# Kernel optimization log

Measured on AMD Instinct MI355X. Metric: run time of the kernel, lower is better.

Reference implementation:

```python
import jax, jax.numpy as jnp
import numpy as np

N = 16384; T = 65536; H = 128; G = 512; E = 65536; NEI = 32768
NIT = 4  # num_interactions
NL = 4   # finaldepth (hidden layers after the first)
EPS = 1e-5
INV = float(1.0 / np.sqrt(1.0 + EPS))  # fresh BatchNorm1d in eval mode: running_mean=0, running_var=1


def _bn(x, g, b):
    # eval-mode BatchNorm with mean=0, var=1: (x - 0)/sqrt(1+eps)*gamma + beta
    return x * (g * INV) + b


def setup_inputs() -> dict:
    key = jax.random.key(0)
    ks = jax.random.split(key, 16)
    inp = {}
    inp["node_positions"] = jax.random.normal(ks[0], (N, 2), jnp.float32)
    inp["edge_index_2rd"] = jax.random.randint(ks[1], (3, T), 0, N)  # (i, j, k) triplets
    inp["edx_jk"] = jax.random.randint(ks[2], (T,), 0, E)
    inp["edx_ij"] = jax.random.randint(ks[3], (T,), 0, E)
    inp["num_edge_inside"] = NEI
    inp["node_to_feature"] = jax.random.randint(ks[4], (N,), 0, G)
    # mlp_geo: Linear(3, H) + BN
    inp["Wg"] = jax.random.normal(ks[5], (3, H), jnp.float32) / np.sqrt(3.0)
    inp["bg"] = jnp.zeros((H,), jnp.float32)
    inp["gamg"] = 1.0 + 0.1 * jax.random.normal(ks[6], (H,), jnp.float32)
    inp["betg"] = 0.1 * jax.random.normal(ks[7], (H,), jnp.float32)
    # per-interaction (NIT), per-edge-type-group (4) MLPs
    inp["W0"] = jax.random.normal(ks[8], (NIT, 4, 4 * H, H), jnp.float32) / np.sqrt(4.0 * H)
    inp["b0"] = jnp.zeros((NIT, 4, H), jnp.float32)
    inp["g0"] = 1.0 + 0.1 * jax.random.normal(ks[9], (NIT, 4, H), jnp.float32)
    inp["be0"] = 0.1 * jax.random.normal(ks[10], (NIT, 4, H), jnp.float32)
    inp["Wh"] = jax.random.normal(ks[11], (NIT, NL, 4, H, H), jnp.float32) / np.sqrt(float(H))
    inp["bh"] = jnp.zeros((NIT, NL, 4, H), jnp.float32)
    inp["gh"] = 1.0 + 0.1 * jax.random.normal(ks[12], (NIT, NL, 4, H), jnp.float32)
    inp["beh"] = 0.1 * jax.random.normal(ks[13], (NIT, NL, 4, H), jnp.float32)
    inp["att"] = jnp.ones((4,), jnp.float32)
    return inp


def reference(node_positions, Wg, bg, gamg, betg, W0, b0, g0, be0, Wh, bh, gh, beh, att,
              edge_index_2rd, edx_jk, edx_ij, num_edge_inside, node_to_feature):
    i, j, k = edge_index_2rd[0], edge_index_2rd[1], edge_index_2rd[2]
    # geometric features of each triplet (i<-j<-k)
    v1 = node_positions[j] - node_positions[i]   # [T,2]
    v2 = node_positions[k] - node_positions[j]   # [T,2]
    d_ij = jnp.linalg.norm(v1, axis=1)
    d_jk = jnp.linalg.norm(v2, axis=1)
    cross = v1[:, 0] * v2[:, 1] - v1[:, 1] * v2[:, 0]
    dot = jnp.sum(v1 * v2, axis=1)
    theta = jnp.arctan2(jnp.abs(cross), dot)
    geo = jnp.stack([d_ij, d_jk, theta], axis=-1)        # [T,3]
    geo = jax.nn.relu(_bn(geo @ Wg + bg, gamg, betg))    # [T,H] geo_encoding

    # 4 mutually exclusive edge-type masks
    in1 = edx_ij < num_edge_inside
    in2 = edx_jk < num_edge_inside
    masks = jnp.stack([in1 & in2, in1 & ~in2, ~in1 & in2, ~in1 & ~in2], axis=0)  # [4,T]
    mask_f = masks.astype(geo.dtype)[:, :, None]         # [4,T,1]

    num_nodes = node_positions.shape[0]
    nf = jnp.zeros((num_nodes, H), geo.dtype)            # input_feature = zeros
    outs = []
    for it in range(NIT):
        x = jnp.concatenate([nf[i], nf[j], nf[k], geo], axis=-1)  # [T,4H]
        h = jnp.einsum('ti,gio->gto', x, W0[it]) + b0[it][:, None, :]
        h = jax.nn.relu(_bn(h, g0[it][:, None, :], be0[it][:, None, :]))
        for l in range(NL):
            h = jnp.einsum('gti,gio->gto', h, Wh[it, l]) + bh[it, l][:, None, :]
            h = jax.nn.relu(_bn(h, gh[it, l][:, None, :], beh[it, l][:, None, :]))
        h = jax.nn.leaky_relu(h, 0.01) * att[:, None, None]       # [4,T,H]
        x_out = jnp.sum(h * mask_f, axis=0)                       # disjoint masks -> select
        nf = jax.ops.segment_sum(x_out, i, num_segments=num_nodes)  # scatter_add over i
        outs.append(nf)
    out = jnp.concatenate(outs, axis=1)                           # [N, NIT*H]
    emb = jax.ops.segment_sum(out, node_to_feature, num_segments=G)  # global_add_pool
    return jnp.minimum(emb, 1.0e6)
```

## Files before the change

### kernel.cpp

```cpp
#include <hip/hip_runtime.h>
#include <hip/hip_bf16.h>
#include <math.h>

#define N_NODES 16384
#define T_TRI   65536
#define H_DIM   128
#define G_POOL  512
#define NITER   4
#define NLAY    4
#define RMAX    (T_TRI + 512)
#define MT      (RMAX / 128)

#define INV_STD 0.9999950000374996f

typedef __attribute__((ext_vector_type(8))) short bhalf8;
typedef __attribute__((ext_vector_type(4))) float f32x4;

__device__ __forceinline__ unsigned short f2b(float f) {
    unsigned int u = __float_as_uint(f);
    unsigned int r = (u + 0x7fffu + ((u >> 16) & 1u)) >> 16;
    return (unsigned short)r;
}
__device__ __forceinline__ float b2f(unsigned short b) {
    return __uint_as_float(((unsigned int)b) << 16);
}


__device__ __forceinline__ int group_of(int eij, int ejk, int nei) {
    return ((eij < nei) ? 0 : 2) + ((ejk < nei) ? 0 : 1);
}

__global__ void histboth_k(const int* __restrict__ edxjk, const int* __restrict__ edxij,
                           const int* __restrict__ neip, const int* __restrict__ eidx,
                           int* __restrict__ ints, int* __restrict__ cnt) {
    __shared__ int lc[4];
    if (threadIdx.x < 4) lc[threadIdx.x] = 0;
    __syncthreads();
    int t = blockIdx.x * 256 + threadIdx.x;
    int nei = *neip;
    int g = group_of(edxij[t], edxjk[t], nei);
    atomicAdd(&lc[g], 1);
    atomicAdd(&cnt[eidx[t]], 1);
    __syncthreads();
    if (threadIdx.x < 4) atomicAdd(&ints[threadIdx.x], lc[threadIdx.x]);
}

__global__ void scanoff_k(int* __restrict__ ints, int* __restrict__ cnt,
                          int* __restrict__ row_start) {
    __shared__ int part[256];
    int tid = threadIdx.x;
    if (tid == 0) {
        int a = 0;
        ints[8] = 0;
        for (int g = 0; g < 4; ++g) {
            a = (a + ints[g] + 127) & ~127;
            ints[9 + g] = a;
        }
    }
    int base = tid * 64;
    int s = 0;
    for (int q = 0; q < 64; ++q) s += cnt[base + q];
    part[tid] = s;
    __syncthreads();
    if (tid == 0) {
        int run = 0;
        for (int q = 0; q < 256; ++q) { int v = part[q]; part[q] = run; run += v; }
        row_start[N_NODES] = run;
    }
    __syncthreads();
    int p = part[tid];
    for (int q = 0; q < 64; ++q) {
        int c = cnt[base + q];
        row_start[base + q] = p;
        cnt[base + q] = p;
        p += c;
    }
}

__global__ void scatboth_k(const int* __restrict__ edxjk, const int* __restrict__ edxij,
                           const int* __restrict__ neip, const int* __restrict__ eidx,
                           int* __restrict__ ints, int* __restrict__ rowmap,
                           int* __restrict__ cursor, int* __restrict__ row_ids) {
    int t = blockIdx.x * 256 + threadIdx.x;
    int nei = *neip;
    int g = group_of(edxij[t], edxjk[t], nei);
    int lane = threadIdx.x & 63;
    unsigned long long msame = 0;
    #pragma unroll
    for (int q = 0; q < 4; ++q) {
        unsigned long long mq = __ballot(g == q);
        if (g == q) msame = mq;
    }
    int leader = __ffsll((long long)msame) - 1;
    int rank = __popcll(msame & ((1ull << lane) - 1ull));
    int base = 0;
    if (lane == leader) base = atomicAdd(&ints[4 + g], __popcll(msame));
    base = __shfl(base, leader);
    int pos = ints[8 + g] + base + rank;
    rowmap[pos] = t;
    int slot = atomicAdd(&cursor[eidx[t]], 1);
    row_ids[slot] = pos;
}


__global__ void t0_k(const float* __restrict__ W0, unsigned short* __restrict__ WT0) {
    __shared__ float t[32][33];
    int b = blockIdx.x;
    int ig = b >> 6;
    int kt = (b >> 2) & 15;
    int nt = b & 3;
    int tx = threadIdx.x & 31, ty = threadIdx.x >> 5;
    const float* src = W0 + ((size_t)ig * 512 + kt * 32) * 128 + nt * 32;
    #pragma unroll
    for (int q = 0; q < 4; ++q) { int r = q * 8 + ty; t[r][tx] = src[(size_t)r * 128 + tx]; }
    __syncthreads();
    unsigned short* dst = WT0 + ((size_t)ig * 128 + nt * 32) * 512 + kt * 32;
    #pragma unroll
    for (int q = 0; q < 4; ++q) { int r = q * 8 + ty; dst[(size_t)r * 512 + tx] = f2b(t[tx][r]); }
}

__global__ void th_k(const float* __restrict__ Wh, unsigned short* __restrict__ WTh) {
    __shared__ float t[32][33];
    int b = blockIdx.x;
    int ilg = b >> 4;
    int kt = (b >> 2) & 3;
    int nt = b & 3;
    int tx = threadIdx.x & 31, ty = threadIdx.x >> 5;
    const float* src = Wh + ((size_t)ilg * 128 + kt * 32) * 128 + nt * 32;
    #pragma unroll
    for (int q = 0; q < 4; ++q) { int r = q * 8 + ty; t[r][tx] = src[(size_t)r * 128 + tx]; }
    __syncthreads();
    unsigned short* dst = WTh + ((size_t)ilg * 128 + nt * 32) * 128 + kt * 32;
    #pragma unroll
    for (int q = 0; q < 4; ++q) { int r = q * 8 + ty; dst[(size_t)r * 128 + tx] = f2b(t[tx][r]); }
}


__global__ void geo_k(const float* __restrict__ pos, const int* __restrict__ eidx,
                      const float* __restrict__ Wg, const float* __restrict__ bg,
                      const float* __restrict__ gamg, const float* __restrict__ betg,
                      unsigned short* __restrict__ geob) {
    int t = blockIdx.x * 16 + (threadIdx.x >> 4);
    int h0 = (threadIdx.x & 15) * 8;
    int ni = eidx[t], nj = eidx[T_TRI + t], nk = eidx[2 * T_TRI + t];
    float ix = pos[2 * ni], iy = pos[2 * ni + 1];
    float jx = pos[2 * nj], jy = pos[2 * nj + 1];
    float kx = pos[2 * nk], ky = pos[2 * nk + 1];
    float v1x = jx - ix, v1y = jy - iy;
    float v2x = kx - jx, v2y = ky - jy;
    float dij = sqrtf(v1x * v1x + v1y * v1y);
    float djk = sqrtf(v2x * v2x + v2y * v2y);
    float cr = v1x * v2y - v1y * v2x;
    float dt = v1x * v2x + v1y * v2y;
    float th = atan2f(fabsf(cr), dt);
    unsigned int ov[4];
    #pragma unroll
    for (int q = 0; q < 4; ++q) {
        unsigned int lo, hi;
        #pragma unroll
        for (int e = 0; e < 2; ++e) {
            int h = h0 + q * 2 + e;
            float v = dij * Wg[h] + djk * Wg[128 + h] + th * Wg[256 + h] + bg[h];
            v = v * (gamg[h] * INV_STD) + betg[h];
            v = fmaxf(v, 0.0f);
            if (e == 0) lo = f2b(v); else hi = f2b(v);
        }
        ov[q] = lo | (hi << 16);
    }
    int4 o = { (int)ov[0], (int)ov[1], (int)ov[2], (int)ov[3] };
    *reinterpret_cast<int4*>(&geob[(size_t)t * 128 + h0]) = o;
}


template<int SKIPNF>
__global__ __launch_bounds__(256, 2) void chain_k(
    const unsigned short* __restrict__ nfb, const unsigned short* __restrict__ geob,
    const int* __restrict__ eidx, const int* __restrict__ rowmap,
    const int* __restrict__ aoff, const unsigned short* __restrict__ WT0,
    const float* __restrict__ b0, const float* __restrict__ g0, const float* __restrict__ be0,
    const unsigned short* __restrict__ WTh,
    const float* __restrict__ bhp, const float* __restrict__ ghp, const float* __restrict__ behp,
    const float* __restrict__ att, unsigned short* __restrict__ hfinal,
    int it) {
    __shared__ unsigned short sh[128 * 128];
    __shared__ unsigned short sw[128 * 128];

    const int r0 = blockIdx.x * 128;
    int g = 0;
    if (r0 >= aoff[1]) g = 1;
    if (r0 >= aoff[2]) g = 2;
    if (r0 >= aoff[3]) g = 3;
    const int tid = threadIdx.x;
    const int lane = tid & 63;
    const int wid = tid >> 6;
    const int wm = wid >> 1, wn = wid & 1;
    const int lr = lane & 15, lq = lane >> 4;

    const int myrow = tid >> 3;
    const int mycolb = (tid & 7) * 8;
    int ttv[4], offi[4], offj[4], offk2[4], offt[4];
    #pragma unroll
    for (int p = 0; p < 4; ++p) {
        int row = p * 32 + myrow;
        int tt = rowmap[r0 + row];
        ttv[p] = tt;
        int ts = tt < 0 ? 0 : tt;
        offt[p] = ts * 128;
        if (!SKIPNF) {
            offi[p]  = eidx[ts] * 128;
            offj[p]  = eidx[T_TRI + ts] * 128;
            offk2[p] = eidx[2 * T_TRI + ts] * 128;
        }
    }

    f32x4 acc[4][4];
    const f32x4 zero4 = {0.f, 0.f, 0.f, 0.f};
    #pragma unroll
    for (int m = 0; m < 4; ++m)
        #pragma unroll
        for (int n = 0; n < 4; ++n) acc[m][n] = zero4;

    const unsigned short* Wt = WT0 + (size_t)(it * 4 + g) * 128 * 512;
    constexpr int KSTEPS = SKIPNF ? 2 : 8;
    constexpr int KBASE  = SKIPNF ? 384 : 0;
    unsigned short* bufs[2] = { sw, sh };
    int4 ra[4], rb[4];

    {
        const int k0 = KBASE;
        const int region = k0 >> 7, half = k0 & 127;
        #pragma unroll
        for (int p = 0; p < 4; ++p) {
            int4 v = {0, 0, 0, 0};
            if (ttv[p] >= 0) {
                const unsigned short* src =
                    region == 0 ? nfb + offi[p] :
                    region == 1 ? nfb + offj[p] :
                    region == 2 ? nfb + offk2[p] :
                                  geob + offt[p];
                v = *reinterpret_cast<const int4*>(src + half + mycolb);
            }
            ra[p] = v;
            rb[p] = *reinterpret_cast<const int4*>(Wt + (size_t)(p * 32 + myrow) * 512 + k0 + mycolb);
        }
        #pragma unroll
        for (int p = 0; p < 4; ++p) {
            int row = p * 32 + myrow;
            int sz = (((tid & 7) ^ (row & 7)) << 3);
            *reinterpret_cast<int4*>(&bufs[0][row * 64 + sz]) = ra[p];
            *reinterpret_cast<int4*>(&bufs[0][128 * 64 + row * 64 + sz]) = rb[p];
        }
        __syncthreads();
    }

    #pragma unroll
    for (int s = 0; s < KSTEPS; ++s) {
        const int cur = s & 1;
        if (s + 1 < KSTEPS) {
            const int k1 = KBASE + (s + 1) * 64;
            const int region = k1 >> 7, half = k1 & 127;
            #pragma unroll
            for (int p = 0; p < 4; ++p) {
                int4 v = {0, 0, 0, 0};
                if (ttv[p] >= 0) {
                    const unsigned short* src =
                        region == 0 ? nfb + offi[p] :
                        region == 1 ? nfb + offj[p] :
                        region == 2 ? nfb + offk2[p] :
                                      geob + offt[p];
                    v = *reinterpret_cast<const int4*>(src + half + mycolb);
                }
                ra[p] = v;
                rb[p] = *reinterpret_cast<const int4*>(Wt + (size_t)(p * 32 + myrow) * 512 + k1 + mycolb);
            }
        }
        const unsigned short* Ab = bufs[cur];
        const unsigned short* Bb = bufs[cur] + 128 * 64;
        #pragma unroll
        for (int ks = 0; ks < 2; ++ks) {
            bhalf8 af[4], bf[4];
            #pragma unroll
            for (int m = 0; m < 4; ++m) {
                int row = 64 * wm + 16 * m + lr;
                int c8 = (4 * ks + lq) ^ (row & 7);
                af[m] = *reinterpret_cast<const bhalf8*>(&Ab[row * 64 + (c8 << 3)]);
            }
            #pragma unroll
            for (int n = 0; n < 4; ++n) {
                int nn = 64 * wn + 16 * n + lr;
                int c8 = (4 * ks + lq) ^ (nn & 7);
                bf[n] = *reinterpret_cast<const bhalf8*>(&Bb[nn * 64 + (c8 << 3)]);
            }
            #pragma unroll
            for (int m = 0; m < 4; ++m)
                #pragma unroll
                for (int n = 0; n < 4; ++n)
                    acc[m][n] = __builtin_amdgcn_mfma_f32_16x16x32_bf16(af[m], bf[n], acc[m][n], 0, 0, 0);
        }
        if (s + 1 < KSTEPS) {
            unsigned short* An = bufs[cur ^ 1];
            #pragma unroll
            for (int p = 0; p < 4; ++p) {
                int row = p * 32 + myrow;
                int sz = (((tid & 7) ^ (row & 7)) << 3);
                *reinterpret_cast<int4*>(&An[row * 64 + sz]) = ra[p];
                *reinterpret_cast<int4*>(&An[128 * 64 + row * 64 + sz]) = rb[p];
            }
        }
        __syncthreads();
    }

    int4 wreg[8];
    {
        const unsigned short* Wl = WTh + (size_t)((it * NLAY + 0) * 4 + g) * 128 * 128;
        #pragma unroll
        for (int p = 0; p < 8; ++p) {
            int idx = p * 256 + tid;
            int n = idx >> 4, gd = idx & 15;
            wreg[p] = *reinterpret_cast<const int4*>(Wl + n * 128 + ((gd ^ (n & 7)) << 3));
        }
    }
    {
        const float* bb = b0 + (it * 4 + g) * 128;
        const float* gg = g0 + (it * 4 + g) * 128;
        const float* be = be0 + (it * 4 + g) * 128;
        #pragma unroll
        for (int n = 0; n < 4; ++n) {
            int col = 64 * wn + 16 * n + lr;
            float sc = gg[col] * INV_STD;
            float bbc = bb[col], bec = be[col];
            int gc = col >> 3, cl = col & 7;
            #pragma unroll
            for (int m = 0; m < 4; ++m)
                #pragma unroll
                for (int r = 0; r < 4; ++r) {
                    int row = 64 * wm + 16 * m + 4 * lq + r;
                    float v = fmaxf((acc[m][n][r] + bbc) * sc + bec, 0.0f);
                    sh[row * 128 + ((gc ^ (row & 7)) << 3) + cl] = f2b(v);
                }
        }
    }
    #pragma unroll
    for (int p = 0; p < 8; ++p) {
        int idx = p * 256 + tid;
        *reinterpret_cast<int4*>(&sw[idx * 8]) = wreg[p];
    }
    __syncthreads();

    for (int l = 0; l < NLAY; ++l) {
        if (l + 1 < NLAY) {
            const unsigned short* Wn = WTh + (size_t)((it * NLAY + l + 1) * 4 + g) * 128 * 128;
            #pragma unroll
            for (int p = 0; p < 8; ++p) {
                int idx = p * 256 + tid;
                int n = idx >> 4, gd = idx & 15;
                wreg[p] = *reinterpret_cast<const int4*>(Wn + n * 128 + ((gd ^ (n & 7)) << 3));
            }
        }
        #pragma unroll
        for (int m = 0; m < 4; ++m)
            #pragma unroll
            for (int n = 0; n < 4; ++n) acc[m][n] = zero4;
        #pragma unroll
        for (int kk = 0; kk < 4; ++kk) {
            bhalf8 af[4], bf[4];
            #pragma unroll
            for (int m = 0; m < 4; ++m) {
                int row = 64 * wm + 16 * m + lr;
                int gc = (4 * kk + lq) ^ (row & 7);
                af[m] = *reinterpret_cast<const bhalf8*>(&sh[row * 128 + (gc << 3)]);
            }
            #pragma unroll
            for (int n = 0; n < 4; ++n) {
                int nn = 64 * wn + 16 * n + lr;
                int gc = (4 * kk + lq) ^ (nn & 7);
                bf[n] = *reinterpret_cast<const bhalf8*>(&sw[nn * 128 + (gc << 3)]);
            }
            #pragma unroll
            for (int m = 0; m < 4; ++m)
                #pragma unroll
                for (int n = 0; n < 4; ++n)
                    acc[m][n] = __builtin_amdgcn_mfma_f32_16x16x32_bf16(af[m], bf[n], acc[m][n], 0, 0, 0);
        }
        if (l + 1 < NLAY) {
            __syncthreads();
            const int ilg = (it * NLAY + l) * 4 + g;
            const float* bb = bhp + (size_t)ilg * 128;
            const float* gg = ghp + (size_t)ilg * 128;
            const float* be = behp + (size_t)ilg * 128;
            #pragma unroll
            for (int n = 0; n < 4; ++n) {
                int col = 64 * wn + 16 * n + lr;
                float sc = gg[col] * INV_STD;
                float bbc = bb[col], bec = be[col];
                int gc = col >> 3, cl = col & 7;
                #pragma unroll
                for (int m = 0; m < 4; ++m)
                    #pragma unroll
                    for (int r = 0; r < 4; ++r) {
                        int row = 64 * wm + 16 * m + 4 * lq + r;
                        float v = fmaxf((acc[m][n][r] + bbc) * sc + bec, 0.0f);
                        sh[row * 128 + ((gc ^ (row & 7)) << 3) + cl] = f2b(v);
                    }
            }
            #pragma unroll
            for (int p = 0; p < 8; ++p) {
                int idx = p * 256 + tid;
                *reinterpret_cast<int4*>(&sw[idx * 8]) = wreg[p];
            }
            __syncthreads();
        }
    }

    __syncthreads();
    {
        const int ilg = (it * NLAY + (NLAY - 1)) * 4 + g;
        const float* bb = bhp + (size_t)ilg * 128;
        const float* gg = ghp + (size_t)ilg * 128;
        const float* be = behp + (size_t)ilg * 128;
        float attg = att[g];
        #pragma unroll
        for (int n = 0; n < 4; ++n) {
            int col = 64 * wn + 16 * n + lr;
            float sc = gg[col] * INV_STD;
            float bbc = bb[col], bec = be[col];
            int gc = col >> 3, cl = col & 7;
            #pragma unroll
            for (int m = 0; m < 4; ++m)
                #pragma unroll
                for (int r = 0; r < 4; ++r) {
                    int row = 64 * wm + 16 * m + 4 * lq + r;
                    float v = fmaxf((acc[m][n][r] + bbc) * sc + bec, 0.0f) * attg;
                    sh[row * 128 + ((gc ^ (row & 7)) << 3) + cl] = f2b(v);
                }
        }
    }
    __syncthreads();
    #pragma unroll
    for (int p = 0; p < 8; ++p) {
        int idx = p * 256 + tid;
        int row = idx >> 4, gd = idx & 15;
        int4 v = *reinterpret_cast<const int4*>(&sh[row * 128 + ((gd ^ (row & 7)) << 3)]);
        *reinterpret_cast<int4*>(&hfinal[(size_t)(r0 + row) * 128 + gd * 8]) = v;
    }
}


__global__ void reduce_k(const unsigned short* __restrict__ hfinal,
                         const int* __restrict__ row_start, const int* __restrict__ row_ids,
                         const int* __restrict__ ntf, unsigned short* __restrict__ nfb,
                         float* __restrict__ emb, int itoff) {
    int n = blockIdx.x * 2 + (threadIdx.x >> 7);
    int c = threadIdx.x & 127;
    int s = row_start[n], e = row_start[n + 1];
    float acc = 0.0f;
    for (int r = s; r < e; ++r) {
        int rid = row_ids[r];
        acc += b2f(hfinal[(size_t)rid * 128 + c]);
    }
    nfb[(size_t)n * 128 + c] = f2b(acc);
    atomicAdd(&emb[(size_t)ntf[n] * 512 + itoff + c], acc);
}

__global__ void clamp_k(const float* __restrict__ emb, float* __restrict__ out) {
    int i = blockIdx.x * 256 + threadIdx.x;
    out[i] = fminf(emb[i], 1.0e6f);
}


extern "C" void kernel_launch(void* const* d_in, const int* in_sizes, int n_in,
                              void* d_out, int out_size, void* d_ws, size_t ws_size,
                              hipStream_t stream) {
    (void)in_sizes; (void)n_in; (void)out_size; (void)ws_size;
    const float* pos   = (const float*)d_in[0];
    const int*   eidx  = (const int*)d_in[1];
    const int*   edxjk = (const int*)d_in[2];
    const int*   edxij = (const int*)d_in[3];
    const int*   neip  = (const int*)d_in[4];
    const int*   ntf   = (const int*)d_in[5];
    const float* Wg    = (const float*)d_in[6];
    const float* bg    = (const float*)d_in[7];
    const float* gamg  = (const float*)d_in[8];
    const float* betg  = (const float*)d_in[9];
    const float* W0    = (const float*)d_in[10];
    const float* b0    = (const float*)d_in[11];
    const float* g0    = (const float*)d_in[12];
    const float* be0   = (const float*)d_in[13];
    const float* Wh    = (const float*)d_in[14];
    const float* bhp   = (const float*)d_in[15];
    const float* ghp   = (const float*)d_in[16];
    const float* behp  = (const float*)d_in[17];
    const float* att   = (const float*)d_in[18];

    char* w = (char*)d_ws;
    size_t off = 0;
    auto alloc = [&](size_t b) -> char* {
        char* p = w + off;
        off += (b + 255) & ~(size_t)255;
        return p;
    };
    int* ints            = (int*)alloc(256);
    int* rowmap          = (int*)alloc((size_t)RMAX * 4);
    int* cnt             = (int*)alloc((size_t)N_NODES * 4);
    int* row_start       = (int*)alloc((size_t)(N_NODES + 1) * 4);
    int* row_ids         = (int*)alloc((size_t)T_TRI * 4);
    unsigned short* WT0  = (unsigned short*)alloc((size_t)16 * 128 * 512 * 2);
    unsigned short* WTh  = (unsigned short*)alloc((size_t)64 * 128 * 128 * 2);
    unsigned short* geob = (unsigned short*)alloc((size_t)T_TRI * 128 * 2);
    unsigned short* nfb  = (unsigned short*)alloc((size_t)N_NODES * 128 * 2);
    unsigned short* hfin = (unsigned short*)alloc((size_t)RMAX * 128 * 2);
    float* emb           = (float*)alloc((size_t)G_POOL * 512 * 4);

    hipMemsetAsync(ints, 0, 256, stream);
    hipMemsetAsync(rowmap, 0xFF, (size_t)RMAX * 4, stream);
    hipMemsetAsync(cnt, 0, (size_t)N_NODES * 4, stream);
    hipMemsetAsync(emb, 0, (size_t)G_POOL * 512 * 4, stream);

    histboth_k<<<256, 256, 0, stream>>>(edxjk, edxij, neip, eidx, ints, cnt);
    scanoff_k<<<1, 256, 0, stream>>>(ints, cnt, row_start);
    scatboth_k<<<256, 256, 0, stream>>>(edxjk, edxij, neip, eidx, ints, rowmap, cnt, row_ids);
    t0_k<<<1024, 256, 0, stream>>>(W0, WT0);
    th_k<<<1024, 256, 0, stream>>>(Wh, WTh);
    geo_k<<<T_TRI / 16, 256, 0, stream>>>(pos, eidx, Wg, bg, gamg, betg, geob);

    for (int it = 0; it < NITER; ++it) {
        if (it == 0)
            chain_k<1><<<MT, 256, 0, stream>>>(nfb, geob, eidx, rowmap, ints + 8, WT0, b0, g0, be0,
                                               WTh, bhp, ghp, behp, att, hfin, it);
        else
            chain_k<0><<<MT, 256, 0, stream>>>(nfb, geob, eidx, rowmap, ints + 8, WT0, b0, g0, be0,
                                               WTh, bhp, ghp, behp, att, hfin, it);
        reduce_k<<<N_NODES / 2, 256, 0, stream>>>(hfin, row_start, row_ids, ntf, nfb, emb, it * 128);
    }

    clamp_k<<<1024, 256, 0, stream>>>(emb, (float*)d_out);
}
```

Baseline: 488.5 us.

## Halve chain kernel row tile and stream weight fragments from global memory

```diff
diff --git a/kernel.cpp b/kernel.cpp
--- a/kernel.cpp
+++ b/kernel.cpp
@@ -9,7 +9,7 @@
 #define NITER   4
 #define NLAY    4
 #define RMAX    (T_TRI + 512)
-#define MT      (RMAX / 128)
+#define MT64    (RMAX / 64)
 
 #define INV_STD 0.9999950000374996f
 
@@ -156,7 +156,7 @@
     unsigned int ov[4];
     #pragma unroll
     for (int q = 0; q < 4; ++q) {
-        unsigned int lo, hi;
+        unsigned int lo = 0, hi = 0;
         #pragma unroll
         for (int e = 0; e < 2; ++e) {
             int h = h0 + q * 2 + e;
@@ -173,7 +173,7 @@
 
 
 template<int SKIPNF>
-__global__ __launch_bounds__(256, 2) void chain_k(
+__global__ __launch_bounds__(256, 4) void chain_k(
     const unsigned short* __restrict__ nfb, const unsigned short* __restrict__ geob,
     const int* __restrict__ eidx, const int* __restrict__ rowmap,
     const int* __restrict__ aoff, const unsigned short* __restrict__ WT0,
@@ -182,25 +182,24 @@
     const float* __restrict__ bhp, const float* __restrict__ ghp, const float* __restrict__ behp,
     const float* __restrict__ att, unsigned short* __restrict__ hfinal,
     int it) {
-    __shared__ unsigned short sh[128 * 128];
-    __shared__ unsigned short sw[128 * 128];
-
-    const int r0 = blockIdx.x * 128;
+    __shared__ unsigned short sh[64 * 128];
+    __shared__ unsigned short sa[2][64 * 64];
+
+    const int r0 = blockIdx.x * 64;
     int g = 0;
     if (r0 >= aoff[1]) g = 1;
     if (r0 >= aoff[2]) g = 2;
     if (r0 >= aoff[3]) g = 3;
     const int tid = threadIdx.x;
     const int lane = tid & 63;
-    const int wid = tid >> 6;
-    const int wm = wid >> 1, wn = wid & 1;
+    const int w = tid >> 6;
     const int lr = lane & 15, lq = lane >> 4;
 
     const int myrow = tid >> 3;
     const int mycolb = (tid & 7) * 8;
-    int ttv[4], offi[4], offj[4], offk2[4], offt[4];
-    #pragma unroll
-    for (int p = 0; p < 4; ++p) {
+    int ttv[2], offi[2], offj[2], offk2[2], offt[2];
+    #pragma unroll
+    for (int p = 0; p < 2; ++p) {
         int row = p * 32 + myrow;
         int tt = rowmap[r0 + row];
         ttv[p] = tt;
@@ -213,24 +212,23 @@
         }
     }
 
-    f32x4 acc[4][4];
+    f32x4 acc[4][2];
     const f32x4 zero4 = {0.f, 0.f, 0.f, 0.f};
     #pragma unroll
     for (int m = 0; m < 4; ++m)
         #pragma unroll
-        for (int n = 0; n < 4; ++n) acc[m][n] = zero4;
+        for (int n = 0; n < 2; ++n) acc[m][n] = zero4;
 
     const unsigned short* Wt = WT0 + (size_t)(it * 4 + g) * 128 * 512;
     constexpr int KSTEPS = SKIPNF ? 2 : 8;
     constexpr int KBASE  = SKIPNF ? 384 : 0;
-    unsigned short* bufs[2] = { sw, sh };
-    int4 ra[4], rb[4];
+    int4 ra[2];
 
     {
         const int k0 = KBASE;
         const int region = k0 >> 7, half = k0 & 127;
         #pragma unroll
-        for (int p = 0; p < 4; ++p) {
+        for (int p = 0; p < 2; ++p) {
             int4 v = {0, 0, 0, 0};
             if (ttv[p] >= 0) {
                 const unsigned short* src =
@@ -240,15 +238,8 @@
                                   geob + offt[p];
                 v = *reinterpret_cast<const int4*>(src + half + mycolb);
             }
-            ra[p] = v;
-            rb[p] = *reinterpret_cast<const int4*>(Wt + (size_t)(p * 32 + myrow) * 512 + k0 + mycolb);
-        }
-        #pragma unroll
-        for (int p = 0; p < 4; ++p) {
             int row = p * 32 + myrow;
-            int sz = (((tid & 7) ^ (row & 7)) << 3);
-            *reinterpret_cast<int4*>(&bufs[0][row * 64 + sz]) = ra[p];
-            *reinterpret_cast<int4*>(&bufs[0][128 * 64 + row * 64 + sz]) = rb[p];
+            *reinterpret_cast<int4*>(&sa[0][row * 64 + (((tid & 7) ^ (row & 7)) << 3)]) = v;
         }
         __syncthreads();
     }
@@ -256,11 +247,12 @@
     #pragma unroll
     for (int s = 0; s < KSTEPS; ++s) {
         const int cur = s & 1;
+        const int k0 = KBASE + s * 64;
         if (s + 1 < KSTEPS) {
-            const int k1 = KBASE + (s + 1) * 64;
+            const int k1 = k0 + 64;
             const int region = k1 >> 7, half = k1 & 127;
             #pragma unroll
-            for (int p = 0; p < 4; ++p) {
+            for (int p = 0; p < 2; ++p) {
                 int4 v = {0, 0, 0, 0};
                 if (ttv[p] >= 0) {
                     const unsigned short* src =
@@ -271,62 +263,48 @@
                     v = *reinterpret_cast<const int4*>(src + half + mycolb);
                 }
                 ra[p] = v;
-                rb[p] = *reinterpret_cast<const int4*>(Wt + (size_t)(p * 32 + myrow) * 512 + k1 + mycolb);
-            }
-        }
-        const unsigned short* Ab = bufs[cur];
-        const unsigned short* Bb = bufs[cur] + 128 * 64;
+            }
+        }
+        bhalf8 rbf[2][2];
+        #pragma unroll
+        for (int n = 0; n < 2; ++n) {
+            int nn = 32 * w + 16 * n + lr;
+            #pragma unroll
+            for (int ks = 0; ks < 2; ++ks)
+                rbf[n][ks] = *reinterpret_cast<const bhalf8*>(Wt + (size_t)nn * 512 + k0 + ks * 32 + lq * 8);
+        }
         #pragma unroll
         for (int ks = 0; ks < 2; ++ks) {
-            bhalf8 af[4], bf[4];
+            bhalf8 af[4];
             #pragma unroll
             for (int m = 0; m < 4; ++m) {
-                int row = 64 * wm + 16 * m + lr;
+                int row = 16 * m + lr;
                 int c8 = (4 * ks + lq) ^ (row & 7);
-                af[m] = *reinterpret_cast<const bhalf8*>(&Ab[row * 64 + (c8 << 3)]);
-            }
-            #pragma unroll
-            for (int n = 0; n < 4; ++n) {
-                int nn = 64 * wn + 16 * n + lr;
-                int c8 = (4 * ks + lq) ^ (nn & 7);
-                bf[n] = *reinterpret_cast<const bhalf8*>(&Bb[nn * 64 + (c8 << 3)]);
+                af[m] = *reinterpret_cast<const bhalf8*>(&sa[cur][row * 64 + (c8 << 3)]);
             }
             #pragma unroll
             for (int m = 0; m < 4; ++m)
                 #pragma unroll
-                for (int n = 0; n < 4; ++n)
-                    acc[m][n] = __builtin_amdgcn_mfma_f32_16x16x32_bf16(af[m], bf[n], acc[m][n], 0, 0, 0);
+                for (int n = 0; n < 2; ++n)
+                    acc[m][n] = __builtin_amdgcn_mfma_f32_16x16x32_bf16(af[m], rbf[n][ks], acc[m][n], 0, 0, 0);
         }
         if (s + 1 < KSTEPS) {
-            unsigned short* An = bufs[cur ^ 1];
-            #pragma unroll
-            for (int p = 0; p < 4; ++p) {
+            #pragma unroll
+            for (int p = 0; p < 2; ++p) {
                 int row = p * 32 + myrow;
-                int sz = (((tid & 7) ^ (row & 7)) << 3);
-                *reinterpret_cast<int4*>(&An[row * 64 + sz]) = ra[p];
-                *reinterpret_cast<int4*>(&An[128 * 64 + row * 64 + sz]) = rb[p];
+                *reinterpret_cast<int4*>(&sa[cur ^ 1][row * 64 + (((tid & 7) ^ (row & 7)) << 3)]) = ra[p];
             }
         }
         __syncthreads();
     }
 
-    int4 wreg[8];
-    {
-        const unsigned short* Wl = WTh + (size_t)((it * NLAY + 0) * 4 + g) * 128 * 128;
-        #pragma unroll
-        for (int p = 0; p < 8; ++p) {
-            int idx = p * 256 + tid;
-            int n = idx >> 4, gd = idx & 15;
-            wreg[p] = *reinterpret_cast<const int4*>(Wl + n * 128 + ((gd ^ (n & 7)) << 3));
-        }
-    }
     {
         const float* bb = b0 + (it * 4 + g) * 128;
         const float* gg = g0 + (it * 4 + g) * 128;
         const float* be = be0 + (it * 4 + g) * 128;
         #pragma unroll
-        for (int n = 0; n < 4; ++n) {
-            int col = 64 * wn + 16 * n + lr;
+        for (int n = 0; n < 2; ++n) {
+            int col = 32 * w + 16 * n + lr;
             float sc = gg[col] * INV_STD;
             float bbc = bb[col], bec = be[col];
             int gc = col >> 3, cl = col & 7;
@@ -334,63 +312,49 @@
             for (int m = 0; m < 4; ++m)
                 #pragma unroll
                 for (int r = 0; r < 4; ++r) {
-                    int row = 64 * wm + 16 * m + 4 * lq + r;
+                    int row = 16 * m + 4 * lq + r;
                     float v = fmaxf((acc[m][n][r] + bbc) * sc + bec, 0.0f);
                     sh[row * 128 + ((gc ^ (row & 7)) << 3) + cl] = f2b(v);
                 }
         }
     }
-    #pragma unroll
-    for (int p = 0; p < 8; ++p) {
-        int idx = p * 256 + tid;
-        *reinterpret_cast<int4*>(&sw[idx * 8]) = wreg[p];
-    }
     __syncthreads();
 
     for (int l = 0; l < NLAY; ++l) {
-        if (l + 1 < NLAY) {
-            const unsigned short* Wn = WTh + (size_t)((it * NLAY + l + 1) * 4 + g) * 128 * 128;
-            #pragma unroll
-            for (int p = 0; p < 8; ++p) {
-                int idx = p * 256 + tid;
-                int n = idx >> 4, gd = idx & 15;
-                wreg[p] = *reinterpret_cast<const int4*>(Wn + n * 128 + ((gd ^ (n & 7)) << 3));
-            }
-        }
+        const unsigned short* Wl = WTh + (size_t)((it * NLAY + l) * 4 + g) * 128 * 128;
         #pragma unroll
         for (int m = 0; m < 4; ++m)
             #pragma unroll
-            for (int n = 0; n < 4; ++n) acc[m][n] = zero4;
+            for (int n = 0; n < 2; ++n) acc[m][n] = zero4;
         #pragma unroll
         for (int kk = 0; kk < 4; ++kk) {
-            bhalf8 af[4], bf[4];
+            bhalf8 af[4], bf[2];
+            #pragma unroll
+            for (int n = 0; n < 2; ++n) {
+                int nn = 32 * w + 16 * n + lr;
+                bf[n] = *reinterpret_cast<const bhalf8*>(Wl + (size_t)nn * 128 + kk * 32 + lq * 8);
+            }
             #pragma unroll
             for (int m = 0; m < 4; ++m) {
-                int row = 64 * wm + 16 * m + lr;
+                int row = 16 * m + lr;
                 int gc = (4 * kk + lq) ^ (row & 7);
                 af[m] = *reinterpret_cast<const bhalf8*>(&sh[row * 128 + (gc << 3)]);
             }
             #pragma unroll
-            for (int n = 0; n < 4; ++n) {
-                int nn = 64 * wn + 16 * n + lr;
-                int gc = (4 * kk + lq) ^ (nn & 7);
-                bf[n] = *reinterpret_cast<const bhalf8*>(&sw[nn * 128 + (gc << 3)]);
-            }
-            #pragma unroll
             for (int m = 0; m < 4; ++m)
                 #pragma unroll
-                for (int n = 0; n < 4; ++n)
+                for (int n = 0; n < 2; ++n)
                     acc[m][n] = __builtin_amdgcn_mfma_f32_16x16x32_bf16(af[m], bf[n], acc[m][n], 0, 0, 0);
         }
+        __syncthreads();
         if (l + 1 < NLAY) {
-            __syncthreads();
             const int ilg = (it * NLAY + l) * 4 + g;
             const float* bb = bhp + (size_t)ilg * 128;
             const float* gg = ghp + (size_t)ilg * 128;
             const float* be = behp + (size_t)ilg * 128;
             #pragma unroll
-            for (int n = 0; n < 4; ++n) {
-                int col = 64 * wn + 16 * n + lr;
+            for (int n = 0; n < 2; ++n) {
+                int col = 32 * w + 16 * n + lr;
                 float sc = gg[col] * INV_STD;
                 float bbc = bb[col], bec = be[col];
                 int gc = col >> 3, cl = col & 7;
@@ -398,21 +362,15 @@
                 for (int m = 0; m < 4; ++m)
                     #pragma unroll
                     for (int r = 0; r < 4; ++r) {
-                        int row = 64 * wm + 16 * m + 4 * lq + r;
+                        int row = 16 * m + 4 * lq + r;
                         float v = fmaxf((acc[m][n][r] + bbc) * sc + bec, 0.0f);
                         sh[row * 128 + ((gc ^ (row & 7)) << 3) + cl] = f2b(v);
                     }
             }
-            #pragma unroll
-            for (int p = 0; p < 8; ++p) {
-                int idx = p * 256 + tid;
-                *reinterpret_cast<int4*>(&sw[idx * 8]) = wreg[p];
-            }
             __syncthreads();
         }
     }
 
-    __syncthreads();
     {
         const int ilg = (it * NLAY + (NLAY - 1)) * 4 + g;
         const float* bb = bhp + (size_t)ilg * 128;
@@ -420,8 +378,8 @@
         const float* be = behp + (size_t)ilg * 128;
         float attg = att[g];
         #pragma unroll
-        for (int n = 0; n < 4; ++n) {
-            int col = 64 * wn + 16 * n + lr;
+        for (int n = 0; n < 2; ++n) {
+            int col = 32 * w + 16 * n + lr;
             float sc = gg[col] * INV_STD;
             float bbc = bb[col], bec = be[col];
             int gc = col >> 3, cl = col & 7;
@@ -429,7 +387,7 @@
             for (int m = 0; m < 4; ++m)
                 #pragma unroll
                 for (int r = 0; r < 4; ++r) {
-                    int row = 64 * wm + 16 * m + 4 * lq + r;
+                    int row = 16 * m + 4 * lq + r;
                     float v = fmaxf((acc[m][n][r] + bbc) * sc + bec, 0.0f) * attg;
                     sh[row * 128 + ((gc ^ (row & 7)) << 3) + cl] = f2b(v);
                 }
@@ -437,7 +395,7 @@
     }
     __syncthreads();
     #pragma unroll
-    for (int p = 0; p < 8; ++p) {
+    for (int p = 0; p < 4; ++p) {
         int idx = p * 256 + tid;
         int row = idx >> 4, gd = idx & 15;
         int4 v = *reinterpret_cast<const int4*>(&sh[row * 128 + ((gd ^ (row & 7)) << 3)]);
@@ -525,11 +483,11 @@
 
     for (int it = 0; it < NITER; ++it) {
         if (it == 0)
-            chain_k<1><<<MT, 256, 0, stream>>>(nfb, geob, eidx, rowmap, ints + 8, WT0, b0, g0, be0,
-                                               WTh, bhp, ghp, behp, att, hfin, it);
+            chain_k<1><<<MT64, 256, 0, stream>>>(nfb, geob, eidx, rowmap, ints + 8, WT0, b0, g0, be0,
+                                                 WTh, bhp, ghp, behp, att, hfin, it);
         else
-            chain_k<0><<<MT, 256, 0, stream>>>(nfb, geob, eidx, rowmap, ints + 8, WT0, b0, g0, be0,
-                                               WTh, bhp, ghp, behp, att, hfin, it);
+            chain_k<0><<<MT64, 256, 0, stream>>>(nfb, geob, eidx, rowmap, ints + 8, WT0, b0, g0, be0,
+                                                 WTh, bhp, ghp, behp, att, hfin, it);
         reduce_k<<<N_NODES / 2, 256, 0, stream>>>(hfin, row_start, row_ids, ntf, nfb, emb, it * 128);
     }
 
```

New measurement: 445.2 us. 1.1x faster.
